# Optimization experiments

Measured on AMD Instinct MI355X. Metric: run time of the kernel, lower is better.

Reference implementation:

```python
import jax, jax.numpy as jnp
import numpy as np

B = 128
IN = 256
NLVL = 6
KLVL = 3
CH = 4
C = 4 * CH * CH          # 64 channels per node
OU = 8                   # out_filter_siz_u
OV = 8                   # out_filter_siz_v
NK = 2 ** KLVL           # 8 leaf nodes per axis
W_SCALE = 1.0 / 16.0     # ~1/sqrt(2*2*C) so 7 stacked relu-convs stay numerically sane


def setup_inputs() -> dict:
    key = jax.random.key(0)
    ks = jax.random.split(key, 2 * NLVL + 4)
    fx = IN // 2 ** NLVL  # 4: input patch filter size
    inp = {}
    inp["in_data"] = jax.random.normal(ks[0], (B, IN, IN, 1), jnp.float32)
    inp["in_filter"] = jax.random.normal(ks[1], (fx, fx, 1, C), jnp.float32) * W_SCALE
    inp["in_bias"] = jnp.zeros((C,), jnp.float32)
    i = 2
    for lvl in range(1, NLVL + 1):
        n = 2 ** min(lvl, KLVL)  # node grid: grows to 2^klvl then stays
        inp[f"f{lvl}"] = jax.random.normal(ks[i], (n, n, 2, 2, C, C), jnp.float32) * W_SCALE
        inp[f"b{lvl}"] = jnp.zeros((n, n, C), jnp.float32)
        i += 1
    inp["Wd"] = jax.random.normal(ks[i], (NK, NK, 2, C, OU * OV), jnp.float32) * W_SCALE
    return inp


def _node_conv(x, w, b):
    # x: [Nu,Nv,B,H,W,C]; w: [Nu,Nv,2,2,C,C]; 2x2 stride-2 VALID conv per node
    Nu, Nv, Bn, H, W, Cc = x.shape
    xr = x.reshape(Nu, Nv, Bn, H // 2, 2, W // 2, 2, Cc)
    y = jnp.einsum('uvbhxwyc,uvxyco->uvbhwo', xr, w)
    return jax.nn.relu(y + b[:, :, None, None, None, :])


def _forward(in_data, in_filter, in_bias, fs, bs, Wd):
    Bn = in_data.shape[0]
    fx, fy = in_filter.shape[0], in_filter.shape[1]
    # input interp conv: stride == kernel -> non-overlapping patch GEMM
    xr = in_data[..., 0].reshape(Bn, in_data.shape[1] // fx, fx, in_data.shape[2] // fy, fy)
    x = jax.nn.relu(jnp.einsum('bxpyq,pqc->bxyc', xr, in_filter[:, :, 0, :]) + in_bias)
    x = x[None, None]  # [1,1,B,2^nlvl,2^nlvl,C] node grid
    for lvl in range(1, NLVL + 1):
        if lvl <= KLVL:
            # children (itu,itv) read parent (itu//2, itv//2)
            x = jnp.repeat(jnp.repeat(x, 2, axis=0), 2, axis=1)
        x = _node_conv(x, fs[lvl - 1], bs[lvl - 1])
    feats = x[:, :, :, 0, 0, :]  # [NK,NK,B,C]; spatial is 1x1 at level nlvl
    out = jnp.einsum('uvbc,uvrck->uvbrk', feats, Wd)  # r in {real, imag}
    out = out.reshape(NK, NK, Bn, 2, OU, OV)
    out = jnp.transpose(out, (2, 0, 4, 1, 5, 3))  # [B,itu,ou,itv,ov,2]
    return out.reshape(Bn, NK * OU, NK * OV, 2)


def reference(in_data, in_filter, in_bias, f1, b1, f2, b2, f3, b3, f4, b4, f5, b5, f6, b6, Wd):
    fs = (f1, f2, f3, f4, f5, f6)
    bs = (b1, b2, b3, b4, b5, b6)
    return _forward(in_data, in_filter, in_bias, fs, bs, Wd)
```

## Files before the change

### kernel.cpp

```cpp
#include <hip/hip_runtime.h>
#include <hip/hip_bf16.h>
#include <cstdint>
#include <cstddef>


typedef __attribute__((ext_vector_type(8))) short short8;
typedef __attribute__((ext_vector_type(4))) float f32x4;
typedef unsigned short ushort_t;

static __device__ __forceinline__ float b2f(const __hip_bfloat16 x) {
    return __bfloat162float(x);
}
static __device__ __forceinline__ ushort_t f2bf(float x) {
    __hip_bfloat16 h = __float2bfloat16(x);
    ushort_t u;
    __builtin_memcpy(&u, &h, 2);
    return u;
}
static __device__ __forceinline__ void gl_lds16(const void* g, void* l) {
    __builtin_amdgcn_global_load_lds(
        (const __attribute__((address_space(1))) void*)g,
        (__attribute__((address_space(3))) void*)l, 16, 0, 0);
}
#define WAIT_LGKM0() __builtin_amdgcn_s_waitcnt(0xC07F)
#define WAIT_VM0()   __builtin_amdgcn_s_waitcnt(0x0F70)

#define PREP_BLOCKS 2533

static __device__ __forceinline__ void prep_work(
    int gid, int isbf,
    const void* f1, const void* f2, const void* f3,
    const void* f4, const void* f5, const void* f6, const void* wdsrc,
    const void* b1, const void* b2, const void* b3,
    const void* b4, const void* b5, const void* b6,
    ushort_t* __restrict__ wbuf, ushort_t* __restrict__ wdbuf,
    float* __restrict__ bbuf)
{
    if (gid >= 648448) return;
    if (gid >= 630784) {
        const int bg = gid - 630784;
        const void* src; int base;
        if      (bg <   256) { src = b1; base = 0;     }
        else if (bg <  1280) { src = b2; base = 256;   }
        else if (bg <  5376) { src = b3; base = 1280;  }
        else if (bg <  9472) { src = b4; base = 5376;  }
        else if (bg < 13568) { src = b5; base = 9472;  }
        else                 { src = b6; base = 13568; }
        const int local = bg - base;
        bbuf[bg] = isbf ? b2f(((const __hip_bfloat16*)src)[local])
                        : ((const float*)src)[local];
        return;
    }
    if (gid >= 565248) {
        const int local = gid - 565248;
        const int lane = local & 63;
        const int slot = (local >> 6) & 15;
        const int site = local >> 10;
        const int ks2 = slot >> 3, nh = slot & 7, q = lane >> 4;
        const int n = nh * 16 + (lane & 15);
        const int r = n >> 6, kk = n & 63;
        const int cbase = ks2 * 32 + q * 8;
        ushort_t pk[8];
        if (isbf) {
            const ushort_t* s = (const ushort_t*)wdsrc;
            #pragma unroll
            for (int j = 0; j < 8; j++)
                pk[j] = s[(((size_t)(site * 2 + r) * 64 + cbase + j) * 64) + kk];
        } else {
            const float* s = (const float*)wdsrc;
            #pragma unroll
            for (int j = 0; j < 8; j++)
                pk[j] = f2bf(s[(((size_t)(site * 2 + r) * 64 + cbase + j) * 64) + kk]);
        }
        *(uint4*)&wdbuf[(size_t)local * 8] = *(uint4*)pk;
        return;
    }
    const void* fsrc; int base;
    if      (gid <   8192) { fsrc = f1; base = 0;      }
    else if (gid <  40960) { fsrc = f2; base = 8192;   }
    else if (gid < 172032) { fsrc = f3; base = 40960;  }
    else if (gid < 303104) { fsrc = f4; base = 172032; }
    else if (gid < 434176) { fsrc = f5; base = 303104; }
    else                   { fsrc = f6; base = 434176; }
    const int local = gid - base;
    const int lane = local & 63;
    const int slot = (local >> 6) & 7;
    const int sitetap = local >> 9;
    const int ks = slot >> 2, nh = slot & 3, q = lane >> 4;
    const int n = (lane & 15) + nh * 16;
    const int kbase = ks * 32 + q * 8;
    ushort_t pk[8];
    if (isbf) {
        const ushort_t* s = (const ushort_t*)fsrc + (size_t)sitetap * 4096;
        #pragma unroll
        for (int j = 0; j < 8; j++) pk[j] = s[(kbase + j) * 64 + n];
    } else {
        const float* s = (const float*)fsrc + (size_t)sitetap * 4096;
        #pragma unroll
        for (int j = 0; j < 8; j++) pk[j] = f2bf(s[(kbase + j) * 64 + n]);
    }
    *(uint4*)&wbuf[(size_t)gid * 8] = *(uint4*)pk;
}

static __device__ __forceinline__ void stage0_body(
    int blk, int isbf,
    const void* __restrict__ in_data, const void* __restrict__ filt,
    const void* __restrict__ bias, __hip_bfloat16* __restrict__ x0,
    int b_off, int Bc)
{
    const int X  = blk & 63;
    const int bl = blk >> 6;
    const int bg = bl + b_off;

    __shared__ float sIn[4][256];
    __shared__ float sF[16][64];
    __shared__ float sB[64];

    const int t = threadIdx.x;
    const size_t srow = ((size_t)bg * 256 + (size_t)X * 4) * 256;

    if (isbf) {
        const __hip_bfloat16* src = (const __hip_bfloat16*)in_data + srow;
        #pragma unroll
        for (int i = 0; i < 4; i++) {
            int flat = i * 256 + t;
            int p = flat >> 8, col = flat & 255;
            sIn[p][col] = b2f(src[(size_t)p * 256 + col]);
        }
        const __hip_bfloat16* fsrc = (const __hip_bfloat16*)filt;
        #pragma unroll
        for (int i = 0; i < 4; i++) {
            int flat = i * 256 + t;
            sF[flat >> 6][flat & 63] = b2f(fsrc[flat]);
        }
        if (t < 64) sB[t] = b2f(((const __hip_bfloat16*)bias)[t]);
    } else {
        const float* src = (const float*)in_data + srow;
        const int p = t >> 6, c4 = (t & 63) * 4;
        *(float4*)&sIn[p][c4] = *(const float4*)(src + (size_t)p * 256 + c4);
        const float* fsrc = (const float*)filt;
        #pragma unroll
        for (int i = 0; i < 4; i++) {
            int flat = i * 256 + t;
            sF[flat >> 6][flat & 63] = fsrc[flat];
        }
        if (t < 64) sB[t] = ((const float*)bias)[t];
    }
    __syncthreads();

    const int ty = t >> 4;
    const int tc = t & 15;

    float acc[4][4];
    {
        const float4 bv = *(const float4*)&sB[tc * 4];
        #pragma unroll
        for (int yi = 0; yi < 4; yi++) {
            acc[yi][0] = bv.x; acc[yi][1] = bv.y;
            acc[yi][2] = bv.z; acc[yi][3] = bv.w;
        }
    }

    #pragma unroll
    for (int p = 0; p < 4; p++) {
        float4 rin[4], rf[4];
        #pragma unroll
        for (int yi = 0; yi < 4; yi++)
            rin[yi] = *(const float4*)&sIn[p][ty * 16 + yi * 4];
        #pragma unroll
        for (int q = 0; q < 4; q++)
            rf[q] = *(const float4*)&sF[p * 4 + q][tc * 4];
        #pragma unroll
        for (int yi = 0; yi < 4; yi++) {
            #pragma unroll
            for (int q = 0; q < 4; q++) {
                const float a = ((const float*)&rin[yi])[q];
                acc[yi][0] = fmaf(a, rf[q].x, acc[yi][0]);
                acc[yi][1] = fmaf(a, rf[q].y, acc[yi][1]);
                acc[yi][2] = fmaf(a, rf[q].z, acc[yi][2]);
                acc[yi][3] = fmaf(a, rf[q].w, acc[yi][3]);
            }
        }
    }

    ushort_t* dst = (ushort_t*)x0;
    #pragma unroll
    for (int yi = 0; yi < 4; yi++) {
        uint2 pk;
        pk.x = (uint32_t)f2bf(fmaxf(acc[yi][0], 0.f))
             | ((uint32_t)f2bf(fmaxf(acc[yi][1], 0.f)) << 16);
        pk.y = (uint32_t)f2bf(fmaxf(acc[yi][2], 0.f))
             | ((uint32_t)f2bf(fmaxf(acc[yi][3], 0.f)) << 16);
        const int wpos = ty * 4 + yi;
        *(uint2*)(dst + ((size_t)(X * 64 + wpos) * Bc + bl) * 64 + tc * 4) = pk;
    }
}

__global__ __launch_bounds__(256) void k_prep0(
    const void* __restrict__ in_data,
    const void* f1, const void* f2, const void* f3,
    const void* f4, const void* f5, const void* f6, const void* wdsrc,
    const void* b1, const void* b2, const void* b3,
    const void* b4, const void* b5, const void* b6,
    ushort_t* __restrict__ wbuf, ushort_t* __restrict__ wdbuf,
    float* __restrict__ bbuf, int* __restrict__ flag,
    const void* __restrict__ filt, const void* __restrict__ bias0,
    __hip_bfloat16* __restrict__ x0, int Bc)
{
    __shared__ int sflag;
    const int t = threadIdx.x;
    if (t < 64) {
        const float v = __uint_as_float(((const uint32_t*)in_data)[t]);
        const bool plaus = (v == 0.0f) || (fabsf(v) > 1e-8f && fabsf(v) < 1e4f);
        const unsigned long long m = __ballot(plaus);
        if (t == 0) sflag = (__popcll(m) >= 48) ? 0 : 1;
    }
    __syncthreads();
    const int isbf = sflag;

    if (blockIdx.x < PREP_BLOCKS) {
        if (blockIdx.x == 0 && t == 0) *flag = isbf;
        prep_work(blockIdx.x * 256 + t, isbf,
                  f1, f2, f3, f4, f5, f6, wdsrc,
                  b1, b2, b3, b4, b5, b6, wbuf, wdbuf, bbuf);
    } else {
        stage0_body(blockIdx.x - PREP_BLOCKS, isbf, in_data, filt, bias0, x0, 0, Bc);
    }
}

__global__ __launch_bounds__(256) void k_stage0(
    const void* __restrict__ in_data, const void* __restrict__ filt,
    const void* __restrict__ bias, __hip_bfloat16* __restrict__ x0,
    const int* __restrict__ flag, int b_off, int Bc)
{
    stage0_body(blockIdx.x, *flag, in_data, filt, bias, x0, b_off, Bc);
}

__global__ __launch_bounds__(256, 2) void k_fused12(
    const __hip_bfloat16* __restrict__ xin,
    const ushort_t* __restrict__ w1,
    const ushort_t* __restrict__ w2,
    const float* __restrict__ b1, const float* __restrict__ b2,
    __hip_bfloat16* __restrict__ xout,
    int Bc, int mtiles)
{
    __shared__ __align__(16) ushort_t smem[34816];

    int idx = blockIdx.x;
    const int mt = idx % mtiles; idx /= mtiles;
    const int w2p = idx & 15;
    const int h2p = idx >> 4;

    const int t = threadIdx.x;
    const int wave = t >> 6, lane = t & 63;
    const int lm = lane & 15, lq = lane >> 4;

    const size_t pstride = (size_t)Bc * 64;

    {
        int brow = mt * 16 + lm;
        if (brow >= Bc) brow = Bc - 1;
        #pragma unroll
        for (int k = 0; k < 4; k++) {
            const int p = wave * 4 + k;
            const int i = p >> 2, j = p & 3;
            const size_t poff =
                ((size_t)(4 * h2p + i) * 64 + (4 * w2p + j)) * pstride;
            #pragma unroll
            for (int ks = 0; ks < 2; ks++) {
                gl_lds16(xin + poff + (size_t)brow * 64 + ks * 32 + lq * 8,
                         &smem[(p * 2 + ks) * 512]);
            }
        }
    }

    const ushort_t* w1site = w1 + (size_t)wave * 16384 + lane * 8;
    short8 breg[32];
    #pragma unroll
    for (int s = 0; s < 32; s++) breg[s] = *(const short8*)(w1site + s * 512);

    float bv1[4];
    #pragma unroll
    for (int fn = 0; fn < 4; fn++) bv1[fn] = b1[wave * 64 + fn * 16 + lm];

    __syncthreads();

    const f32x4 zero = {0.f, 0.f, 0.f, 0.f};
    ushort_t* l1b = smem + 16384;

    #pragma unroll
    for (int ab = 0; ab < 4; ab++) {
        const int a = ab >> 1, b = ab & 1;
        f32x4 acc[4];
        #pragma unroll
        for (int fn = 0; fn < 4; fn++) acc[fn] = zero;

        #pragma unroll
        for (int cd = 0; cd < 4; cd++) {
            const int p = (2 * a + (cd >> 1)) * 4 + (2 * b + (cd & 1));
            #pragma unroll
            for (int ks = 0; ks < 2; ks++) {
                short8 afr = *(const short8*)&smem[(p * 2 + ks) * 512 + lane * 8];
                #pragma unroll
                for (int fn = 0; fn < 4; fn++)
                    acc[fn] = __builtin_amdgcn_mfma_f32_16x16x32_bf16(
                        afr, breg[cd * 8 + ks * 4 + fn], acc[fn], 0, 0, 0);
            }
        }
        ushort_t* dst = l1b + (wave * 4 + ab) * 1152;
        #pragma unroll
        for (int fn = 0; fn < 4; fn++) {
            #pragma unroll
            for (int r = 0; r < 4; r++) {
                const int m = lq * 4 + r;
                dst[m * 72 + fn * 16 + lm] =
                    f2bf(fmaxf(acc[fn][r] + bv1[fn], 0.f));
            }
        }
    }
    __syncthreads();

    ushort_t* so_buf = smem + wave * 2176;
    for (int k = 0; k < 4; k++) {
        const int s2 = wave * 4 + k;
        const int u2 = s2 >> 2, v2 = s2 & 3;
        const int s1p = (u2 >> 1) * 2 + (v2 >> 1);
        const ushort_t* w2site = w2 + (size_t)s2 * 16384 + lane * 8;

        f32x4 acc[4];
        #pragma unroll
        for (int fn = 0; fn < 4; fn++) acc[fn] = zero;

        #pragma unroll
        for (int ab = 0; ab < 4; ab++) {
            const ushort_t* sl = l1b + (s1p * 4 + ab) * 1152;
            #pragma unroll
            for (int ks = 0; ks < 2; ks++) {
                short8 afr = *(const short8*)&sl[lm * 72 + ks * 32 + lq * 8];
                #pragma unroll
                for (int fn = 0; fn < 4; fn++) {
                    short8 bfr = *(const short8*)(w2site + (ab * 8 + ks * 4 + fn) * 512);
                    acc[fn] = __builtin_amdgcn_mfma_f32_16x16x32_bf16(
                        afr, bfr, acc[fn], 0, 0, 0);
                }
            }
        }

        float bv2[4];
        #pragma unroll
        for (int fn = 0; fn < 4; fn++) bv2[fn] = b2[s2 * 64 + fn * 16 + lm];

        #pragma unroll
        for (int fn = 0; fn < 4; fn++) {
            #pragma unroll
            for (int r = 0; r < 4; r++) {
                const int m = lq * 4 + r;
                so_buf[m * 68 + fn * 16 + lm] =
                    f2bf(fmaxf(acc[fn][r] + bv2[fn], 0.f));
            }
        }
        const size_t obase = ((size_t)s2 * 256 + h2p * 16 + w2p) * pstride;
        #pragma unroll
        for (int i2 = 0; i2 < 2; i2++) {
            const int task = i2 * 64 + lane;
            const int oct = task & 7, row = task >> 3;
            const int brw = mt * 16 + row;
            if (brw < Bc) {
                *(uint4*)(xout + obase + (size_t)brw * 64 + oct * 8) =
                    *(const uint4*)&so_buf[row * 68 + oct * 8];
            }
        }
    }
}

__global__ __launch_bounds__(256, 2) void k_level4(
    const __hip_bfloat16* __restrict__ xin,
    const ushort_t* __restrict__ wbuf,
    const float* __restrict__ bbuf,
    __hip_bfloat16* __restrict__ xout,
    int Nv_out, int HW, int Bc, int mtiles)
{
    __shared__ __align__(16) ushort_t smem[17408];

    int idx = blockIdx.x;
    const int mt = idx % mtiles; idx /= mtiles;
    const int w  = idx % HW; idx /= HW;
    const int h  = idx % HW; idx /= HW;
    const int Nv_in = Nv_out >> 1;
    const int vp = idx % Nv_in;
    const int up = idx / Nv_in;

    const int t = threadIdx.x;
    const int wave = t >> 6, lane = t & 63;
    const int lm = lane & 15, lq = lane >> 4;

    const int so = (2 * up + (wave >> 1)) * Nv_out + (2 * vp + (wave & 1));
    const int H_in = HW * 2;
    const size_t pstride = (size_t)Bc * 64;
    const size_t siteb = (size_t)(up * Nv_in + vp) * H_in * H_in * pstride;
    const ushort_t* wsite = wbuf + (size_t)so * 4 * 4096 + lane * 8;

    {
        const int hi = 2 * h + (wave >> 1), wi = 2 * w + (wave & 1);
        const size_t tapoff = siteb + ((size_t)hi * H_in + wi) * pstride;
        #pragma unroll
        for (int j = 0; j < 8; j++) {
            const int ks = j >> 2, mh = j & 3;
            int b = mt * 64 + mh * 16 + lm;
            if (b >= Bc) b = Bc - 1;
            gl_lds16(xin + tapoff + (size_t)b * 64 + ks * 32 + lq * 8,
                     &smem[(wave * 8 + j) * 512]);
        }
    }

    short8 breg[32];
    #pragma unroll
    for (int s = 0; s < 32; s++)
        breg[s] = *(const short8*)(wsite + s * 512);

    float bv[4];
    #pragma unroll
    for (int fn = 0; fn < 4; fn++) bv[fn] = bbuf[so * 64 + fn * 16 + lm];

    __syncthreads();

    const f32x4 zero = {0.f, 0.f, 0.f, 0.f};
    f32x4 acc[4][4];
    #pragma unroll
    for (int i = 0; i < 4; i++)
        #pragma unroll
        for (int j = 0; j < 4; j++) acc[i][j] = zero;

    #pragma unroll
    for (int tap = 0; tap < 4; tap++) {
        #pragma unroll
        for (int ks = 0; ks < 2; ks++) {
            #pragma unroll
            for (int fm = 0; fm < 4; fm++) {
                short8 a = *(const short8*)&smem[(tap * 8 + ks * 4 + fm) * 512 + lane * 8];
                #pragma unroll
                for (int fn = 0; fn < 4; fn++)
                    acc[fm][fn] = __builtin_amdgcn_mfma_f32_16x16x32_bf16(
                        a, breg[tap * 8 + ks * 4 + fn], acc[fm][fn], 0, 0, 0);
            }
        }
    }
    __syncthreads();

    ushort_t* so_buf = smem + wave * 4352;
    #pragma unroll
    for (int fm = 0; fm < 4; fm++) {
        #pragma unroll
        for (int fn = 0; fn < 4; fn++) {
            #pragma unroll
            for (int r = 0; r < 4; r++) {
                const int row = fm * 16 + lq * 4 + r;
                so_buf[row * 68 + fn * 16 + lm] =
                    f2bf(fmaxf(acc[fm][fn][r] + bv[fn], 0.f));
            }
        }
    }
    __syncthreads();

    const size_t obase = ((size_t)so * HW * HW + (size_t)h * HW + w) * pstride;
    #pragma unroll
    for (int i = 0; i < 8; i++) {
        const int task = i * 64 + lane;
        const int oct = task & 7, row = task >> 3;
        const int b = mt * 64 + row;
        if (b < Bc) {
            *(uint4*)(xout + obase + (size_t)b * 64 + oct * 8) =
                *(const uint4*)&so_buf[row * 68 + oct * 8];
        }
    }
}

__global__ __launch_bounds__(256) void k_f456(
    const __hip_bfloat16* __restrict__ xin,
    const ushort_t* __restrict__ w4, const ushort_t* __restrict__ w5,
    const ushort_t* __restrict__ w6, const ushort_t* __restrict__ wd,
    const float* __restrict__ b4, const float* __restrict__ b5,
    const float* __restrict__ b6,
    void* __restrict__ out, const int* __restrict__ flag,
    int Bc, int b_off, int mtiles)
{
    const int isbf = *flag;
    const int bx = blockIdx.x;
    const int mt = bx % mtiles;
    const int site = bx / mtiles;
    const int u = site >> 3, v = site & 7;

    __shared__ __align__(16) ushort_t smem[37376];

    const int t = threadIdx.x;
    const int wv = t >> 6, lane = t & 63;
    const int lm = lane & 15, lq = lane >> 4;

    const ushort_t* w6s = w6 + (size_t)site * 16384 + lane * 8;
    const ushort_t* wds = wd + (size_t)site * 8192  + lane * 8;

    float bv4[4], bv5[4];
    #pragma unroll
    for (int fn = 0; fn < 4; fn++) {
        bv4[fn] = b4[site * 64 + fn * 16 + lm];
        bv5[fn] = b5[site * 64 + fn * 16 + lm];
    }
    const float bv6 = b6[site * 64 + wv * 16 + lm];

    {
        const ushort_t* w4s = w4 + (size_t)site * 16384;
        #pragma unroll
        for (int s2 = 0; s2 < 8; s2++) {
            const int s = wv * 8 + s2;
            gl_lds16(w4s + s * 512 + lane * 8, &smem[s * 512]);
        }
    }
    __syncthreads();

    const f32x4 zero = {0.f, 0.f, 0.f, 0.f};
    const int h5 = wv >> 1, w5p = wv & 1;
    ushort_t* mid1w = smem + 16384 + wv * 4224;
    ushort_t* Aw = smem + 33280 + wv * 1024;
    const size_t pstride = (size_t)Bc * 64;

    int brow = mt * 16 + lm;
    if (brow >= Bc) brow = Bc - 1;
    const __hip_bfloat16* xbase =
        xin + (size_t)site * 64 * pstride + (size_t)brow * 64 + lq * 8;

    for (int i = 0; i < 4; i++) {
        const int h4 = 2 * h5 + (i >> 1), w4p = 2 * w5p + (i & 1);
        f32x4 acc[4];
        #pragma unroll
        for (int b_ = 0; b_ < 4; b_++) acc[b_] = zero;

        for (int tap = 0; tap < 4; tap++) {
            const int h3 = 2 * h4 + (tap >> 1), w3 = 2 * w4p + (tap & 1);
            const size_t poff = (size_t)(h3 * 8 + w3) * pstride;
            WAIT_LGKM0();
            #pragma unroll
            for (int ks = 0; ks < 2; ks++) {
                gl_lds16(xbase + poff + ks * 32, &Aw[ks * 512]);
            }
            WAIT_VM0();
            __builtin_amdgcn_sched_barrier(0);
            #pragma unroll
            for (int ks = 0; ks < 2; ks++) {
                short8 a = *(const short8*)&Aw[ks * 512 + lane * 8];
                #pragma unroll
                for (int fn = 0; fn < 4; fn++) {
                    short8 bfr = *(const short8*)&smem[(tap * 8 + ks * 4 + fn) * 512 + lane * 8];
                    acc[fn] = __builtin_amdgcn_mfma_f32_16x16x32_bf16(a, bfr, acc[fn], 0, 0, 0);
                }
            }
        }
        #pragma unroll
        for (int fn = 0; fn < 4; fn++) {
            #pragma unroll
            for (int r = 0; r < 4; r++) {
                const int m = lq * 4 + r;
                const int ch = fn * 16 + lm;
                mid1w[m * 264 + i * 64 + ch] =
                    f2bf(fmaxf(acc[fn][r] + bv4[fn], 0.f));
            }
        }
    }
    __syncthreads();

    {
        const ushort_t* w5s = w5 + (size_t)site * 16384;
        #pragma unroll
        for (int s2 = 0; s2 < 8; s2++) {
            const int s = wv * 8 + s2;
            gl_lds16(w5s + s * 512 + lane * 8, &smem[s * 512]);
        }
    }
    __syncthreads();

    short8 b3r[8];
    short8 wdr[4];
    {
        f32x4 acc2[4];
        #pragma unroll
        for (int b_ = 0; b_ < 4; b_++) acc2[b_] = zero;

        #pragma unroll
        for (int i = 0; i < 4; i++) {
            #pragma unroll
            for (int ks = 0; ks < 2; ks++) {
                short8 a0 = *(const short8*)&mid1w[lm * 264 + i * 64 + ks * 32 + lq * 8];
                #pragma unroll
                for (int fn = 0; fn < 4; fn++) {
                    short8 bfr = *(const short8*)&smem[(i * 8 + ks * 4 + fn) * 512 + lane * 8];
                    acc2[fn] = __builtin_amdgcn_mfma_f32_16x16x32_bf16(a0, bfr, acc2[fn], 0, 0, 0);
                }
            }
        }

        #pragma unroll
        for (int tap = 0; tap < 4; tap++)
            #pragma unroll
            for (int ks = 0; ks < 2; ks++)
                b3r[tap * 2 + ks] = *(const short8*)(w6s + (tap * 8 + ks * 4 + wv) * 512);
        #pragma unroll
        for (int ks = 0; ks < 2; ks++)
            #pragma unroll
            for (int n2 = 0; n2 < 2; n2++)
                wdr[ks * 2 + n2] = *(const short8*)(wds + (ks * 8 + 2 * wv + n2) * 512);

        #pragma unroll
        for (int fn = 0; fn < 4; fn++) {
            #pragma unroll
            for (int r = 0; r < 4; r++) {
                const int m = lq * 4 + r;
                const int ch = fn * 16 + lm;
                mid1w[m * 72 + ch] =
                    f2bf(fmaxf(acc2[fn][r] + bv5[fn], 0.f));
            }
        }
    }
    __syncthreads();

    {
        f32x4 acc3 = zero;
        #pragma unroll
        for (int tap = 0; tap < 4; tap++) {
            const ushort_t* sl = smem + 16384 + tap * 4224;
            #pragma unroll
            for (int ks = 0; ks < 2; ks++) {
                short8 a0 = *(const short8*)&sl[lm * 72 + ks * 32 + lq * 8];
                acc3 = __builtin_amdgcn_mfma_f32_16x16x32_bf16(a0, b3r[tap * 2 + ks], acc3, 0, 0, 0);
            }
        }
        ushort_t* mid3 = smem + 33280;
        #pragma unroll
        for (int r = 0; r < 4; r++) {
            const int m = lq * 4 + r;
            const int ch = wv * 16 + lm;
            mid3[m * 72 + ch] = f2bf(fmaxf(acc3[r] + bv6, 0.f));
        }
    }
    __syncthreads();

    {
        const ushort_t* mid3 = smem + 33280;
        f32x4 acc4[2];
        acc4[0] = zero; acc4[1] = zero;
        #pragma unroll
        for (int ks = 0; ks < 2; ks++) {
            short8 a0 = *(const short8*)&mid3[lm * 72 + ks * 32 + lq * 8];
            #pragma unroll
            for (int n2 = 0; n2 < 2; n2++) {
                acc4[n2] = __builtin_amdgcn_mfma_f32_16x16x32_bf16(a0, wdr[ks * 2 + n2], acc4[n2], 0, 0, 0);
            }
        }
        #pragma unroll
        for (int n2 = 0; n2 < 2; n2++) {
            const int n = (2 * wv + n2) * 16 + lm;
            const int rr = n >> 6, ou = (n >> 3) & 7, ov = n & 7;
            const size_t obase =
                (((size_t)(u * 8 + ou)) * 64 + (v * 8 + ov)) * 2 + rr;
            #pragma unroll
            for (int reg = 0; reg < 4; reg++) {
                const int brw = mt * 16 + lq * 4 + reg;
                if (brw < Bc) {
                    const size_t oidx = obase + (size_t)(b_off + brw) * 8192;
                    if (isbf) ((__hip_bfloat16*)out)[oidx] =
                        __float2bfloat16(acc4[n2][reg]);
                    else ((float*)out)[oidx] = acc4[n2][reg];
                }
            }
        }
    }
}

extern "C" void kernel_launch(void* const* d_in, const int* in_sizes, int n_in,
                              void* d_out, int out_size, void* d_ws, size_t ws_size,
                              hipStream_t stream)
{
    (void)in_sizes; (void)n_in; (void)out_size;

    const void* in_data = d_in[0];
    const void* filt    = d_in[1];
    const void* bias0   = d_in[2];
    const void* fl[7];
    const void* bl[7];
    for (int l = 1; l <= 6; l++) {
        fl[l] = d_in[1 + 2 * l];
        bl[l] = d_in[2 + 2 * l];
    }
    const void* Wd = d_in[15];

    const int Bfull = 128;
    const size_t perB = (size_t)64 * 64 * 64;

    const size_t wbufBytes  = 565248ull * 16;
    const size_t wdbufBytes = 65536ull * 16;
    const size_t bbufBytes  = 17664ull * 4;
    const size_t headBytes  = 256 + wbufBytes + wdbufBytes + bbufBytes;

    const size_t avail = ws_size > headBytes ? ws_size - headBytes : 0;
    int Bc = 0;
    for (int c = 128; c >= 1; c >>= 1) {
        if ((size_t)2 * c * perB * sizeof(__hip_bfloat16) <= avail) { Bc = c; break; }
    }
    if (Bc == 0) return;

    int* flag = (int*)d_ws;
    ushort_t* wbuf  = (ushort_t*)((char*)d_ws + 256);
    ushort_t* wdbuf = (ushort_t*)((char*)d_ws + 256 + wbufBytes);
    float* bbuf = (float*)((char*)d_ws + 256 + wbufBytes + wdbufBytes);
    __hip_bfloat16* bufA = (__hip_bfloat16*)((char*)d_ws + headBytes);
    __hip_bfloat16* bufB = bufA + (size_t)Bc * perB;

    const int mt4  = (Bc + 63) / 64;
    const int mt16 = (Bc + 15) / 16;

    for (int b_off = 0; b_off < Bfull; b_off += Bc) {
        if (b_off == 0) {
            k_prep0<<<dim3(PREP_BLOCKS + Bc * 64), 256, 0, stream>>>(
                in_data,
                fl[1], fl[2], fl[3], fl[4], fl[5], fl[6], Wd,
                bl[1], bl[2], bl[3], bl[4], bl[5], bl[6],
                wbuf, wdbuf, bbuf, flag,
                filt, bias0, bufA, Bc);
        } else {
            k_stage0<<<dim3(Bc * 64), 256, 0, stream>>>(in_data, filt, bias0, bufA, flag, b_off, Bc);
        }

        k_fused12<<<dim3(256 * mt16), 256, 0, stream>>>(
            bufA, wbuf, wbuf + 65536, bbuf, bbuf + 256, bufB, Bc, mt16);

        {
            dim3 grid(4 * 4 * 8 * 8 * mt4);
            k_level4<<<grid, 256, 0, stream>>>(bufB, wbuf + 327680,
                bbuf + 1280, bufA, 8, 8, Bc, mt4);
        }

        k_f456<<<dim3(64 * mt16), 256, 0, stream>>>(bufA,
            wbuf + 1376256, wbuf + 2424832, wbuf + 3473408, wdbuf,
            bbuf + 5376, bbuf + 9472, bbuf + 13568,
            d_out, flag, Bc, b_off, mt16);
    }
}
```

Baseline: 248.8 us.

## Remap fused level-1/2 blocks to a parent node and preload level-2 weights into registers

k_fused12 now assigns each block one parent node and a strip of four output positions, instead of one position across all nodes. Each wave keeps a single node's level-1 weights and a single level-2 child's weights in registers for the whole block and loops over four spatial positions. Previously the level-2 weights were re-read from global memory for every MFMA. The aim is to remove repeated global weight fetches and reuse weight registers across positions, at the cost of more syncthreads, serialised input loads per position and higher register pressure; sched_barriers are added to pin the weight-load ordering.

```diff
diff --git a/kernel.cpp b/kernel.cpp
--- a/kernel.cpp
+++ b/kernel.cpp
@@ -248,8 +248,10 @@
 
     int idx = blockIdx.x;
     const int mt = idx % mtiles; idx /= mtiles;
-    const int w2p = idx & 15;
-    const int h2p = idx >> 4;
+    const int parent = idx & 3; idx >>= 2;
+    const int wstrip = idx & 3;
+    const int h2p = idx >> 2;
+    const int ip = parent >> 1, jp = parent & 1;
 
     const int t = threadIdx.x;
     const int wave = t >> 6, lane = t & 63;
@@ -257,57 +259,57 @@
 
     const size_t pstride = (size_t)Bc * 64;
 
-    {
-        int brow = mt * 16 + lm;
-        if (brow >= Bc) brow = Bc - 1;
+    int brow = mt * 16 + lm;
+    if (brow >= Bc) brow = Bc - 1;
+
+    const ushort_t* w1site = w1 + (size_t)parent * 16384 + lane * 8;
+    short8 breg[32];
+    #pragma unroll
+    for (int s = 0; s < 32; s++) breg[s] = *(const short8*)(w1site + s * 512);
+    __builtin_amdgcn_sched_barrier(0);
+
+    float bv1[4];
+    #pragma unroll
+    for (int fn = 0; fn < 4; fn++) bv1[fn] = b1[parent * 64 + fn * 16 + lm];
+
+    const f32x4 zero = {0.f, 0.f, 0.f, 0.f};
+    ushort_t* l1b = smem + 16384;
+    const int wa = wave >> 1, wb = wave & 1;
+
+    for (int pos = 0; pos < 4; pos++) {
+        const int w2p = wstrip * 4 + pos;
+        __syncthreads();
+
         #pragma unroll
         for (int k = 0; k < 4; k++) {
-            const int p = wave * 4 + k;
-            const int i = p >> 2, j = p & 3;
+            const int lpos = wave * 4 + k;
+            const int i0 = lpos >> 2, j0 = lpos & 3;
             const size_t poff =
-                ((size_t)(4 * h2p + i) * 64 + (4 * w2p + j)) * pstride;
+                ((size_t)(4 * h2p + i0) * 64 + (4 * w2p + j0)) * pstride;
             #pragma unroll
             for (int ks = 0; ks < 2; ks++) {
                 gl_lds16(xin + poff + (size_t)brow * 64 + ks * 32 + lq * 8,
-                         &smem[(p * 2 + ks) * 512]);
-            }
-        }
-    }
-
-    const ushort_t* w1site = w1 + (size_t)wave * 16384 + lane * 8;
-    short8 breg[32];
-    #pragma unroll
-    for (int s = 0; s < 32; s++) breg[s] = *(const short8*)(w1site + s * 512);
-
-    float bv1[4];
-    #pragma unroll
-    for (int fn = 0; fn < 4; fn++) bv1[fn] = b1[wave * 64 + fn * 16 + lm];
-
-    __syncthreads();
-
-    const f32x4 zero = {0.f, 0.f, 0.f, 0.f};
-    ushort_t* l1b = smem + 16384;
-
-    #pragma unroll
-    for (int ab = 0; ab < 4; ab++) {
-        const int a = ab >> 1, b = ab & 1;
+                         &smem[(lpos * 2 + ks) * 512]);
+            }
+        }
+        __syncthreads();
+
         f32x4 acc[4];
         #pragma unroll
         for (int fn = 0; fn < 4; fn++) acc[fn] = zero;
-
         #pragma unroll
         for (int cd = 0; cd < 4; cd++) {
-            const int p = (2 * a + (cd >> 1)) * 4 + (2 * b + (cd & 1));
+            const int lpos = (2 * wa + (cd >> 1)) * 4 + (2 * wb + (cd & 1));
             #pragma unroll
             for (int ks = 0; ks < 2; ks++) {
-                short8 afr = *(const short8*)&smem[(p * 2 + ks) * 512 + lane * 8];
+                short8 afr = *(const short8*)&smem[(lpos * 2 + ks) * 512 + lane * 8];
                 #pragma unroll
                 for (int fn = 0; fn < 4; fn++)
                     acc[fn] = __builtin_amdgcn_mfma_f32_16x16x32_bf16(
                         afr, breg[cd * 8 + ks * 4 + fn], acc[fn], 0, 0, 0);
             }
         }
-        ushort_t* dst = l1b + (wave * 4 + ab) * 1152;
+        ushort_t* dst = l1b + (pos * 4 + wave) * 1152;
         #pragma unroll
         for (int fn = 0; fn < 4; fn++) {
             #pragma unroll
@@ -320,54 +322,59 @@
     }
     __syncthreads();
 
-    ushort_t* so_buf = smem + wave * 2176;
-    for (int k = 0; k < 4; k++) {
-        const int s2 = wave * 4 + k;
-        const int u2 = s2 >> 2, v2 = s2 & 3;
-        const int s1p = (u2 >> 1) * 2 + (v2 >> 1);
+    {
+        const int di = wave >> 1, dj = wave & 1;
+        const int s2 = (2 * ip + di) * 4 + (2 * jp + dj);
         const ushort_t* w2site = w2 + (size_t)s2 * 16384 + lane * 8;
-
-        f32x4 acc[4];
-        #pragma unroll
-        for (int fn = 0; fn < 4; fn++) acc[fn] = zero;
-
-        #pragma unroll
-        for (int ab = 0; ab < 4; ab++) {
-            const ushort_t* sl = l1b + (s1p * 4 + ab) * 1152;
-            #pragma unroll
-            for (int ks = 0; ks < 2; ks++) {
-                short8 afr = *(const short8*)&sl[lm * 72 + ks * 32 + lq * 8];
+        short8 wreg[32];
+        #pragma unroll
+        for (int s = 0; s < 32; s++) wreg[s] = *(const short8*)(w2site + s * 512);
+        __builtin_amdgcn_sched_barrier(0);
+
+        float bv2[4];
+        #pragma unroll
+        for (int fn = 0; fn < 4; fn++) bv2[fn] = b2[s2 * 64 + fn * 16 + lm];
+
+        ushort_t* so_buf = smem + wave * 2176;
+
+        for (int pos = 0; pos < 4; pos++) {
+            const int w2p = wstrip * 4 + pos;
+            f32x4 acc[4];
+            #pragma unroll
+            for (int fn = 0; fn < 4; fn++) acc[fn] = zero;
+
+            #pragma unroll
+            for (int ab = 0; ab < 4; ab++) {
+                const ushort_t* sl = l1b + (pos * 4 + ab) * 1152;
                 #pragma unroll
-                for (int fn = 0; fn < 4; fn++) {
-                    short8 bfr = *(const short8*)(w2site + (ab * 8 + ks * 4 + fn) * 512);
-                    acc[fn] = __builtin_amdgcn_mfma_f32_16x16x32_bf16(
-                        afr, bfr, acc[fn], 0, 0, 0);
+                for (int ks = 0; ks < 2; ks++) {
+                    short8 afr = *(const short8*)&sl[lm * 72 + ks * 32 + lq * 8];
+                    #pragma unroll
+                    for (int fn = 0; fn < 4; fn++)
+                        acc[fn] = __builtin_amdgcn_mfma_f32_16x16x32_bf16(
+                            afr, wreg[ab * 8 + ks * 4 + fn], acc[fn], 0, 0, 0);
                 }
             }
-        }
-
-        float bv2[4];
-        #pragma unroll
-        for (int fn = 0; fn < 4; fn++) bv2[fn] = b2[s2 * 64 + fn * 16 + lm];
-
-        #pragma unroll
-        for (int fn = 0; fn < 4; fn++) {
-            #pragma unroll
-            for (int r = 0; r < 4; r++) {
-                const int m = lq * 4 + r;
-                so_buf[m * 68 + fn * 16 + lm] =
-                    f2bf(fmaxf(acc[fn][r] + bv2[fn], 0.f));
-            }
-        }
-        const size_t obase = ((size_t)s2 * 256 + h2p * 16 + w2p) * pstride;
-        #pragma unroll
-        for (int i2 = 0; i2 < 2; i2++) {
-            const int task = i2 * 64 + lane;
-            const int oct = task & 7, row = task >> 3;
-            const int brw = mt * 16 + row;
-            if (brw < Bc) {
-                *(uint4*)(xout + obase + (size_t)brw * 64 + oct * 8) =
-                    *(const uint4*)&so_buf[row * 68 + oct * 8];
+
+            #pragma unroll
+            for (int fn = 0; fn < 4; fn++) {
+                #pragma unroll
+                for (int r = 0; r < 4; r++) {
+                    const int m = lq * 4 + r;
+                    so_buf[m * 68 + fn * 16 + lm] =
+                        f2bf(fmaxf(acc[fn][r] + bv2[fn], 0.f));
+                }
+            }
+            const size_t obase = ((size_t)s2 * 256 + h2p * 16 + w2p) * pstride;
+            #pragma unroll
+            for (int i2 = 0; i2 < 2; i2++) {
+                const int task = i2 * 64 + lane;
+                const int oct = task & 7, row = task >> 3;
+                const int brw = mt * 16 + row;
+                if (brw < Bc) {
+                    *(uint4*)(xout + obase + (size_t)brw * 64 + oct * 8) =
+                        *(const uint4*)&so_buf[row * 68 + oct * 8];
+                }
             }
         }
     }
@@ -417,6 +424,7 @@
     #pragma unroll
     for (int s = 0; s < 32; s++)
         breg[s] = *(const short8*)(wsite + s * 512);
+    __builtin_amdgcn_sched_barrier(0);
 
     float bv[4];
     #pragma unroll
```

Result: faster. 243.0 us (-2.4%).
